# Performance work log

Hardware: AMD Instinct MI355X
Metric: run time of the kernel (lower is better)

The kernel has to match this reference:

```python
import jax, jax.numpy as jnp
import numpy as np

BN_EPS = 1e-5

def _sqdist(a, b):
    # a: (B,N,3), b: (B,M,3) -> (B,N,M)
    return (jnp.sum(a**2, -1)[:, :, None] + jnp.sum(b**2, -1)[:, None, :]
            - 2.0 * jnp.einsum('bnc,bmc->bnm', a, b))

def _knn_idx(pts, k):
    # smallest-k neighbor indices, (B,N,k)
    d = _sqdist(pts, pts)
    _, idx = jax.lax.top_k(-d, k)
    return idx

def _group(feat, idx):
    # feat (B,C,N), idx (B,N,K) -> (B,C,N,K)
    return jax.vmap(lambda f, i: f[:, i])(feat, idx)

def _gather_pts(pts, idx):
    # pts (B,M,C), idx (B,...) -> (B,...,C)
    return jax.vmap(lambda p, i: p[i])(pts, idx)

def _conv1(w, b, x):
    # 1x1 conv1d: w (O,C), x (B,C,N)
    return jnp.einsum('oc,bcn->bon', w, x) + b[None, :, None]

def _conv2(w, x, b=None):
    # 1x1 conv2d: w (O,C), x (B,C,N,K)
    y = jnp.einsum('oc,bcnk->bonk', w, x)
    return y if b is None else y + b[None, :, None, None]

def _bn_eval(x, gamma, beta):
    # eval-mode BatchNorm2d with running_mean=0, running_var=1
    s = gamma / jnp.sqrt(1.0 + BN_EPS)
    return x * s[None, :, None, None] + beta[None, :, None, None]

def _lgrp(x_q, x, P_anchor, map_idx, anchor_dist, lw1, lw2, lw3, k=16):
    # x_q, x: (B,n,3) -> weights (B,dim,n,k)
    d = _sqdist(x_q, x)
    _, idx = jax.lax.top_k(-d, k)                      # (B,n,k)
    neighbors = _gather_pts(x, idx)                    # (B,n,k,3)
    R1 = jnp.abs(x_q[:, :, None, :] - neighbors)       # (B,n,k,3)
    B_idx = _gather_pts(map_idx[..., None], idx)[..., 0]  # (B,n,k)
    anchorA = _gather_pts(P_anchor, map_idx)           # (B,n,3)
    anchorB = _gather_pts(P_anchor, B_idx)             # (B,n,k,3)
    dA = jnp.linalg.norm(x_q - anchorA, axis=-1)       # (B,n)
    dB = jnp.linalg.norm(neighbors - anchorB, axis=-1) # (B,n,k)
    dAB = jax.vmap(lambda ad, a, bi: ad[a[:, None], bi])(anchor_dist, map_idx, B_idx)
    R2s = dA[:, :, None] + dAB + dB                    # (B,n,k)
    R2 = jnp.broadcast_to(R2s[..., None], R1.shape)
    feats = jnp.concatenate([R1, R2], axis=-1).transpose(0, 3, 1, 2)  # (B,6,n,k)
    h = jax.nn.relu(_conv2(lw1, feats))
    h = jax.nn.relu(_conv2(lw2, h))
    return _conv2(lw3, h)                              # (B,dim,n,k)

def setup_inputs() -> dict:
    key = jax.random.key(0)
    ks = jax.random.split(key, 32)
    B, C_in, n, dim, M, k = 2, 128, 2048, 256, 128, 16
    hid_p, hid_a = 64, dim * 4
    s = 0.05
    inp = {
        'x': jax.random.normal(ks[0], (B, C_in, n), jnp.float32),
        'pos': jax.random.normal(ks[1], (B, 3, n), jnp.float32),
        'fps_idx': jax.random.randint(ks[2], (B, n), 0, n),
        'P_anchor': jax.random.normal(ks[3], (B, M, 3), jnp.float32),
        'map_idx': jax.random.randint(ks[4], (B, n), 0, M),
        'anchor_dist': jax.random.uniform(ks[5], (B, M, M), jnp.float32) * 2.0,
        'w_start': jax.random.normal(ks[6], (dim, C_in)) * s,
        'b_start': jnp.zeros((dim,), jnp.float32),
        'w_key': jax.random.normal(ks[7], (dim, dim)) * s,
        'b_key': jnp.zeros((dim,), jnp.float32),
        'w_query': jax.random.normal(ks[8], (dim, dim)) * s,
        'b_query': jnp.zeros((dim,), jnp.float32),
        'w_value': jax.random.normal(ks[9], (dim, dim)) * s,
        'b_value': jnp.zeros((dim,), jnp.float32),
        'pw1': jax.random.normal(ks[10], (hid_p, 3)) * s,
        'pb1': jnp.zeros((hid_p,), jnp.float32),
        'pg1': jnp.ones((hid_p,), jnp.float32),
        'pbt1': jnp.zeros((hid_p,), jnp.float32),
        'pw2': jax.random.normal(ks[11], (dim, hid_p)) * s,
        'pb2': jnp.zeros((dim,), jnp.float32),
        'lw1': jax.random.normal(ks[12], (32, 6)) * s,
        'lw2': jax.random.normal(ks[13], (64, 32)) * s,
        'lw3': jax.random.normal(ks[14], (dim, 64)) * s,
        'aw1': jax.random.normal(ks[15], (hid_a, dim)) * s,
        'ab1': jnp.zeros((hid_a,), jnp.float32),
        'ag1': jnp.ones((hid_a,), jnp.float32),
        'abt1': jnp.zeros((hid_a,), jnp.float32),
        'aw2': jax.random.normal(ks[16], (dim, hid_a)) * s,
        'ab2': jnp.zeros((dim,), jnp.float32),
        'w_end': jax.random.normal(ks[17], (C_in, dim)) * s,
        'b_end': jnp.zeros((C_in,), jnp.float32),
    }
    return inp

def reference(x, pos, fps_idx, P_anchor, map_idx, anchor_dist,
              w_start, b_start, w_key, b_key, w_query, b_query, w_value, b_value,
              pw1, pb1, pg1, pbt1, pw2, pb2, lw1, lw2, lw3,
              aw1, ab1, ag1, abt1, aw2, ab2, w_end, b_end):
    n_knn = 16
    identity = x
    xf = _conv1(w_start, b_start, x)                   # (B,dim,n)
    pos_f = pos.transpose(0, 2, 1)                     # (B,n,3)
    idx_knn = _knn_idx(pos_f, n_knn)                   # (B,n,k)
    key_f = _conv1(w_key, b_key, xf)
    value = _conv1(w_value, b_value, xf)
    query = _conv1(w_query, b_query, xf)
    key_g = _group(key_f, idx_knn)                     # (B,dim,n,k)
    qk_rel = query[:, :, :, None] - key_g
    pos_rel = pos[:, :, :, None] - _group(pos, idx_knn)
    f_l = _lgrp(pos_f, pos_f, P_anchor, map_idx, anchor_dist, lw1, lw2, lw3, k=16)
    # pos_mlp: conv-bn-relu-conv
    h = _bn_eval(_conv2(pw1, pos_rel, pb1), pg1, pbt1)
    pos_emb = _conv2(pw2, jax.nn.relu(h), pb2)         # (B,dim,n,k)
    # attn_mlp
    a = _bn_eval(_conv2(aw1, qk_rel + pos_emb + f_l, ab1), ag1, abt1)
    attention = _conv2(aw2, jax.nn.relu(a), ab2)
    attention = jax.nn.softmax(attention, axis=-1)
    value_e = value[:, :, :, None] + pos_emb + f_l
    agg = jnp.sum(attention * value_e, axis=-1)        # (B,dim,n)
    y = _conv1(w_end, b_end, agg)
    return y + identity
```

## Files before the change

kernel.cpp:

```cpp
#include <hip/hip_runtime.h>
#include <hip/hip_bf16.h>

typedef __hip_bfloat16 bf16;
typedef unsigned short u16;
typedef __attribute__((ext_vector_type(8))) short s8v;
typedef __attribute__((ext_vector_type(4))) float f32x4;

#define NP    2048
#define DC    256
#define MA    128
#define KNN_  16
#define LKV   768

#define MFMA_B16(a,b,c) __builtin_amdgcn_mfma_f32_16x16x32_bf16(a,b,c,0,0,0)

__device__ __forceinline__ float u2f(u16 u){ return __uint_as_float(((unsigned int)u)<<16); }
__device__ __forceinline__ u16 f2u(float f){ bf16 h=__float2bfloat16(f); u16 us; __builtin_memcpy(&us,&h,2); return us; }

__device__ __forceinline__ s8v ldpk(const u16* pk, int rb, int KS, int ks, int l){
  return *(const s8v*)(pk + (((size_t)((rb*KS + ks)*64 + l))<<3));
}

__device__ __forceinline__ s8v ldF(const u16* base, int cf, int ks, int NKS, int l){
  return *(const s8v*)((const char*)base + (((cf*NKS + ks)<<10) | (l<<4)));
}
__device__ __forceinline__ int faddr(int col, int ch, int NKS){
  int cf = col>>4, ks = ch>>5, lane = (((ch>>3)&3)<<4)|(col&15), j = ch&7;
  return ((cf*NKS + ks)<<10) + (lane<<4) + (j<<1);
}
__device__ __forceinline__ void stF4(u16* base, int col, int ch0, int NKS,
                                     float v0, float v1, float v2, float v3){
  uint2 pkv;
  pkv.x = (unsigned)f2u(v0) | ((unsigned)f2u(v1)<<16);
  pkv.y = (unsigned)f2u(v2) | ((unsigned)f2u(v3)<<16);
  *(uint2*)((char*)base + faddr(col, ch0, NKS)) = pkv;
}
__device__ __forceinline__ void stF1(u16* base, int col, int ch, int NKS, float v){
  *(u16*)((char*)base + faddr(col, ch, NKS)) = f2u(v);
}
__device__ __forceinline__ void ldF4(const u16* base, int col, int ch0, int NKS, float* o){
  uint2 pkv = *(const uint2*)((const char*)base + faddr(col, ch0, NKS));
  o[0] = u2f(pkv.x & 0xffff); o[1] = u2f(pkv.x>>16);
  o[2] = u2f(pkv.y & 0xffff); o[3] = u2f(pkv.y>>16);
}

template<bool XT, bool OT, bool RES>
__global__ __launch_bounds__(256) void mgemm(
    const u16* __restrict__ apk, const float* __restrict__ X,
    const float* __restrict__ bias, const float* __restrict__ resid,
    float* __restrict__ out, int M, int N, int K, int ldo)
{
  __shared__ u16 Bt[64*256];
  const int tid = threadIdx.x;
  const int w = tid>>6, l = tid&63, k = l&15, g = l>>4;
  const int n0 = blockIdx.x*64, m0 = blockIdx.y*128, bb = blockIdx.z;
  const int KS = K >> 5;
  if constexpr (!XT) {
    for (int e = tid*4; e < 64*K; e += 1024) {
      int kk = e >> 6, c = e & 63;
      float4 v = *(const float4*)(X + (size_t)bb*K*N + (size_t)kk*N + n0 + c);
      stF1(Bt, c+0, kk, KS, v.x); stF1(Bt, c+1, kk, KS, v.y);
      stF1(Bt, c+2, kk, KS, v.z); stF1(Bt, c+3, kk, KS, v.w);
    }
  } else {
    for (int e = tid*4; e < 64*256; e += 1024) {
      int c = e >> 8, kk = e & 255;
      float4 v = *(const float4*)(X + ((size_t)bb*N + n0 + c)*256 + kk);
      stF4(Bt, c, kk, KS, v.x, v.y, v.z, v.w);
    }
  }
  __syncthreads();
  f32x4 acc[2][4] = {};
  const int rbase = (m0>>4) + w*2;
  for (int ks = 0; ks < KS; ks++) {
    s8v a0 = ldpk(apk, rbase,   KS, ks, l);
    s8v a1 = ldpk(apk, rbase+1, KS, ks, l);
#pragma unroll
    for (int cf = 0; cf < 4; cf++) {
      s8v bF = ldF(Bt, cf, ks, KS, l);
      acc[0][cf] = MFMA_B16(a0, bF, acc[0][cf]);
      acc[1][cf] = MFMA_B16(a1, bF, acc[1][cf]);
    }
  }
#pragma unroll
  for (int ri = 0; ri < 2; ri++) {
    int mrow = m0 + w*32 + ri*16 + g*4;
#pragma unroll
    for (int r = 0; r < 4; r++) {
      int m = mrow + r;
      float bv = bias[m];
#pragma unroll
      for (int cf = 0; cf < 4; cf++) {
        int n = n0 + cf*16 + k;
        float v = acc[ri][cf][r] + bv;
        if constexpr (RES) v += resid[((size_t)bb*M + m)*N + n];
        if constexpr (OT) out[((size_t)bb*N + n)*ldo + m] = v;
        else              out[((size_t)bb*M + m)*N + n] = v;
      }
    }
  }
}

__global__ __launch_bounds__(1024) void knn_kernel(const float* __restrict__ pos, int* __restrict__ idx)
{
  __shared__ float px[NP], py[NP], pz[NP], pn[NP];
  const int tid = threadIdx.x;
  const int w = tid >> 6, l = tid & 63;
  const int bb = blockIdx.x >> 7;
  const int q0 = (blockIdx.x & 127) * 16;
  const float* pp = pos + (size_t)bb * 3 * NP;
  for (int t = tid; t < NP; t += 1024) {
    float x = pp[t], y = pp[NP + t], z = pp[2*NP + t];
    px[t] = x; py[t] = y; pz[t] = z; pn[t] = x*x + y*y + z*z;
  }
  __syncthreads();
  const int qi = q0 + w;
  const float qx = px[qi], qy = py[qi], qz = pz[qi], qn = pn[qi];
  float bd[16]; int bi[16];
#pragma unroll
  for (int t = 0; t < 16; t++) { bd[t] = 3.4e38f; bi[t] = -1; }
  float worst = 3.4e38f;
  for (int t = 0; t < 32; t++) {
    int j = t*64 + l;
    float d = qn + pn[j] - 2.f * (qx*px[j] + qy*py[j] + qz*pz[j]);
    if (__any(d < worst)) {
      float cd = (d < worst) ? d : 3.4e38f;
      int   cj = j;
#pragma unroll
      for (int s = 0; s < 16; s++) {
        bool sw = cd < bd[s];
        float od = bd[s]; int oj = bi[s];
        bd[s] = sw ? cd : od;  bi[s] = sw ? cj : oj;
        cd    = sw ? od : cd;  cj    = sw ? oj : cj;
      }
      worst = bd[15];
    }
  }
  int myj = 0;
#pragma unroll
  for (int r = 0; r < 16; r++) {
    float md = bd[0]; int mj = bi[0];
#pragma unroll
    for (int o = 1; o < 64; o <<= 1) {
      float od = __shfl_xor(md, o);
      int   oj = __shfl_xor(mj, o);
      bool tk = (od < md) || (od == md && ((unsigned)oj < (unsigned)mj));
      md = tk ? od : md;  mj = tk ? oj : mj;
    }
    if (l == r) myj = mj;
    bool win = (bi[0] == mj);
#pragma unroll
    for (int s = 0; s < 15; s++) {
      bd[s] = win ? bd[s+1] : bd[s];
      bi[s] = win ? bi[s+1] : bi[s];
    }
    bd[15] = win ? 3.4e38f : bd[15];
  }
  if (l < 16) idx[((size_t)bb * NP + qi) * KNN_ + l] = myj;
}

__global__ __launch_bounds__(256) void prep_kernel(
    const float* __restrict__ aw1, const float* __restrict__ aw2,
    const float* __restrict__ lw3, const float* __restrict__ pw2,
    const float* __restrict__ w_start, const float* __restrict__ w_key,
    const float* __restrict__ w_query, const float* __restrict__ w_value,
    const float* __restrict__ w_end,
    const float* __restrict__ b_key, const float* __restrict__ b_query,
    const float* __restrict__ b_value,
    const float* __restrict__ ag1, const float* __restrict__ ab1, const float* __restrict__ abt1,
    const float* __restrict__ pg1, const float* __restrict__ pb1, const float* __restrict__ pbt1,
    u16* __restrict__ aw1pk, u16* __restrict__ aw2pk, u16* __restrict__ wppk,
    u16* __restrict__ wstpk, u16* __restrict__ wkqvpk, u16* __restrict__ wendpk,
    float* __restrict__ sa, float* __restrict__ oa, float* __restrict__ sp,
    float* __restrict__ op_, float* __restrict__ bkqv)
{
  int i = blockIdx.x * 256 + threadIdx.x;
  const float inv = rsqrtf(1.0f + 1e-5f);
  if (i < 262144) {
    int rb = i >> 12, rem = i & 4095, ks = rem >> 9, l = (rem >> 3) & 63, j = rem & 7;
    int row = rb*16 + (l & 15), colk = ks*32 + (l >> 4)*8 + j;
    aw1pk[i] = f2u(aw1[(size_t)row*256 + colk]); return;
  }
  i -= 262144;
  if (i < 262144) {
    int rb = i >> 14, rem = i & 16383, ks = rem >> 9, l = (rem >> 3) & 63, j = rem & 7;
    int row = rb*16 + (l & 15), colk = ks*32 + (l >> 4)*8 + j;
    aw2pk[i] = f2u(aw2[(size_t)row*1024 + colk]); return;
  }
  i -= 262144;
  if (i < 32768) {
    int rb = i >> 11, rem = i & 2047, ks = rem >> 9, l = (rem >> 3) & 63, j = rem & 7;
    int row = rb*16 + (l & 15), colk = ks*32 + (l >> 4)*8 + j;
    float v = (colk < 64) ? lw3[row*64 + colk] : pw2[row*64 + (colk - 64)];
    wppk[i] = f2u(v); return;
  }
  i -= 32768;
  if (i < 32768) {
    int rb = i >> 11, rem = i & 2047, ks = rem >> 9, l = (rem >> 3) & 63, j = rem & 7;
    int row = rb*16 + (l & 15), colk = ks*32 + (l >> 4)*8 + j;
    wstpk[i] = f2u(w_start[(size_t)row*128 + colk]); return;
  }
  i -= 32768;
  if (i < 196608) {
    int rb = i >> 12, rem = i & 4095, ks = rem >> 9, l = (rem >> 3) & 63, j = rem & 7;
    int row = rb*16 + (l & 15), colk = ks*32 + (l >> 4)*8 + j;
    float v = (row < 256) ? w_key[(size_t)row*256 + colk]
            : (row < 512) ? w_query[(size_t)(row-256)*256 + colk]
                          : w_value[(size_t)(row-512)*256 + colk];
    wkqvpk[i] = f2u(v); return;
  }
  i -= 196608;
  if (i < 32768) {
    int rb = i >> 12, rem = i & 4095, ks = rem >> 9, l = (rem >> 3) & 63, j = rem & 7;
    int row = rb*16 + (l & 15), colk = ks*32 + (l >> 4)*8 + j;
    wendpk[i] = f2u(w_end[(size_t)row*256 + colk]); return;
  }
  i -= 32768;
  if (i < 1024) { float s_ = ag1[i]*inv; sa[i] = s_; oa[i] = ab1[i]*s_ + abt1[i]; return; }
  i -= 1024;
  if (i < 64)  { float s_ = pg1[i]*inv; sp[i] = s_; op_[i] = pb1[i]*s_ + pbt1[i]; return; }
  i -= 64;
  if (i < 768) {
    bkqv[i] = (i < 256) ? b_key[i] : (i < 512) ? b_query[i-256] : b_value[i-512];
  }
}

__global__ __launch_bounds__(256, 2) void fused_attn(
    const float* __restrict__ kqv, const int* __restrict__ knn_idx,
    const float* __restrict__ pos, const int* __restrict__ map_idx,
    const float* __restrict__ P_anchor, const float* __restrict__ adist,
    const float* __restrict__ lw1f, const float* __restrict__ lw2f, const float* __restrict__ pw1f,
    const float* __restrict__ spv, const float* __restrict__ opv, const float* __restrict__ pb2f,
    const u16* __restrict__ aw1pk, const float* __restrict__ sav, const float* __restrict__ oav,
    const u16* __restrict__ aw2pk, const u16* __restrict__ wppk, const float* __restrict__ ab2f,
    float* __restrict__ aggT)
{
  __shared__ __align__(16) char smem[65536];
  u16*   s_t   = (u16*)smem;
  u16*   hid0  = (u16*)(smem + 32768);
  u16*   hid1  = (u16*)(smem + 49152);
  float* fFEAT = (float*)smem;
  float* fPREL = (float*)(smem + 1632);
  u16*   fH1   = (u16*) (smem + 2448);

  const int tid = threadIdx.x;
  const int w = tid >> 6, l = tid & 63;
  const int k = l & 15, g = l >> 4;
  const int p0 = blockIdx.x * 4;
  const int b = p0 >> 11, pi0 = p0 & 2047;
  const int pi = pi0 + w;
  const int col_w = w*16 + k;

  const float* kqvB = kqv + (size_t)b * NP * LKV;
  const int* knnB = knn_idx + ((size_t)b * NP) * KNN_;

  if (l < 16) {
    int kk = l;
    int j = knnB[(size_t)pi * KNN_ + kk];
    const float* pp = pos + (size_t)b * 3 * NP;
    float qx = pp[pi], qy = pp[NP+pi], qz = pp[2*NP+pi];
    float nx = pp[j],  ny = pp[NP+j],  nz = pp[2*NP+j];
    float r1x = qx-nx, r1y = qy-ny, r1z = qz-nz;
    fPREL[(w*3+0)*17+kk] = r1x; fPREL[(w*3+1)*17+kk] = r1y; fPREL[(w*3+2)*17+kk] = r1z;
    int mi = map_idx[b*NP + pi];
    int bj = map_idx[b*NP + j];
    const float* pa = P_anchor + (size_t)b * MA * 3;
    float ax = pa[mi*3], ay = pa[mi*3+1], az = pa[mi*3+2];
    float bx = pa[bj*3], by = pa[bj*3+1], bz = pa[bj*3+2];
    float dA = sqrtf((qx-ax)*(qx-ax)+(qy-ay)*(qy-ay)+(qz-az)*(qz-az));
    float dB = sqrtf((nx-bx)*(nx-bx)+(ny-by)*(ny-by)+(nz-bz)*(nz-bz));
    float dAB = adist[(size_t)b*MA*MA + mi*MA + bj];
    float r2 = dA + dAB + dB;
    fFEAT[(w*6+0)*17+kk] = fabsf(r1x); fFEAT[(w*6+1)*17+kk] = fabsf(r1y);
    fFEAT[(w*6+2)*17+kk] = fabsf(r1z);
    fFEAT[(w*6+3)*17+kk] = r2; fFEAT[(w*6+4)*17+kk] = r2; fFEAT[(w*6+5)*17+kk] = r2;
  }
  __syncthreads();

  {
    float f0=fFEAT[(w*6+0)*17+k], f1=fFEAT[(w*6+1)*17+k], f2=fFEAT[(w*6+2)*17+k],
          f3=fFEAT[(w*6+3)*17+k], f4=fFEAT[(w*6+4)*17+k], f5=fFEAT[(w*6+5)*17+k];
#pragma unroll
    for (int jj = 0; jj < 8; jj++) {
      int h = g*8 + jj;
      const float* wp = lw1f + h*6;
      float v = wp[0]*f0 + wp[1]*f1 + wp[2]*f2 + wp[3]*f3 + wp[4]*f4 + wp[5]*f5;
      fH1[(w*32+h)*17+k] = f2u(fmaxf(v, 0.f));
    }
  }
  __syncthreads();

  {
    float hr[32];
#pragma unroll
    for (int t = 0; t < 32; t++) hr[t] = u2f(fH1[(w*32+t)*17+k]);
#pragma unroll
    for (int jj = 0; jj < 16; jj++) {
      int h = g*16 + jj;
      const float4* wp = (const float4*)(lw2f + h*32);
      float a = 0.f;
#pragma unroll
      for (int t4 = 0; t4 < 8; t4++) {
        float4 wv = wp[t4];
        a += wv.x*hr[t4*4] + wv.y*hr[t4*4+1] + wv.z*hr[t4*4+2] + wv.w*hr[t4*4+3];
      }
      stF1(hid0, col_w, h, 4, fmaxf(a, 0.f));
    }
    float pr0 = fPREL[(w*3+0)*17+k], pr1 = fPREL[(w*3+1)*17+k], pr2 = fPREL[(w*3+2)*17+k];
#pragma unroll
    for (int jj = 0; jj < 16; jj++) {
      int h = g*16 + jj;
      float d = pw1f[h*3]*pr0 + pw1f[h*3+1]*pr1 + pw1f[h*3+2]*pr2;
      stF1(hid0, col_w, 64 + h, 4, fmaxf(d*spv[h] + opv[h], 0.f));
    }
  }
  __syncthreads();

  {
    f32x4 accs[4][4];
#pragma unroll
    for (int fr = 0; fr < 4; fr++) {
      int ch0 = w*64 + fr*16 + g*4;
      const float4 p4 = *(const float4*)(pb2f + ch0);
#pragma unroll
      for (int fc = 0; fc < 4; fc++) {
        int j = knnB[(size_t)(pi0 + fc) * KNN_ + k];
        const float4 q4 = *(const float4*)(kqvB + (size_t)(pi0 + fc)*LKV + 256 + ch0);
        const float4 k4 = *(const float4*)(kqvB + (size_t)j*LKV + ch0);
        accs[fr][fc][0] = q4.x - k4.x + p4.x;
        accs[fr][fc][1] = q4.y - k4.y + p4.y;
        accs[fr][fc][2] = q4.z - k4.z + p4.z;
        accs[fr][fc][3] = q4.w - k4.w + p4.w;
      }
    }
#pragma unroll
    for (int ks = 0; ks < 4; ks++) {
      s8v aF[4];
#pragma unroll
      for (int fr = 0; fr < 4; fr++) aF[fr] = ldpk(wppk, w*4 + fr, 4, ks, l);
#pragma unroll
      for (int fc = 0; fc < 4; fc++) {
        s8v bF = ldF(hid0, fc, ks, 4, l);
#pragma unroll
        for (int fr = 0; fr < 4; fr++) accs[fr][fc] = MFMA_B16(aF[fr], bF, accs[fr][fc]);
      }
    }
#pragma unroll
    for (int fr = 0; fr < 4; fr++)
#pragma unroll
      for (int fc = 0; fc < 4; fc++)
        stF4(s_t, fc*16 + k, w*64 + fr*16 + g*4, 8,
             accs[fr][fc][0], accs[fr][fc][1], accs[fr][fc][2], accs[fr][fc][3]);
  }
  __syncthreads();

  f32x4 acc2[4][4];
#pragma unroll
  for (int fr = 0; fr < 4; fr++) {
    const float4 a4 = *(const float4*)(ab2f + w*64 + fr*16 + g*4);
#pragma unroll
    for (int fc = 0; fc < 4; fc++) {
      acc2[fr][fc][0] = a4.x; acc2[fr][fc][1] = a4.y;
      acc2[fr][fc][2] = a4.z; acc2[fr][fc][3] = a4.w;
    }
  }

  {
    f32x4 acc1[2][4] = {};
    const int rb0 = w*2;
#pragma unroll
    for (int ks = 0; ks < 8; ks++) {
      s8v a0 = ldpk(aw1pk, rb0,     8, ks, l);
      s8v a1 = ldpk(aw1pk, rb0 + 1, 8, ks, l);
#pragma unroll
      for (int cf = 0; cf < 4; cf++) {
        s8v bF = ldF(s_t, cf, ks, 8, l);
        acc1[0][cf] = MFMA_B16(a0, bF, acc1[0][cf]);
        acc1[1][cf] = MFMA_B16(a1, bF, acc1[1][cf]);
      }
    }
#pragma unroll
    for (int ri = 0; ri < 2; ri++) {
      int hl = w*32 + ri*16 + g*4;
      const float4 sc = *(const float4*)(sav + hl);
      const float4 of = *(const float4*)(oav + hl);
#pragma unroll
      for (int cf = 0; cf < 4; cf++) {
        float v0 = fmaxf(acc1[ri][cf][0]*sc.x + of.x, 0.f);
        float v1 = fmaxf(acc1[ri][cf][1]*sc.y + of.y, 0.f);
        float v2 = fmaxf(acc1[ri][cf][2]*sc.z + of.z, 0.f);
        float v3 = fmaxf(acc1[ri][cf][3]*sc.w + of.w, 0.f);
        stF4(hid0, cf*16 + k, hl, 4, v0, v1, v2, v3);
      }
    }
  }
  __syncthreads();

  for (int c = 0; c < 8; c++) {
    u16* cur = (c & 1) ? hid1 : hid0;
    u16* nxt = (c & 1) ? hid0 : hid1;
#pragma unroll
    for (int ks = 0; ks < 4; ks++) {
      s8v aF[4];
#pragma unroll
      for (int rf = 0; rf < 4; rf++) aF[rf] = ldpk(aw2pk, w*4 + rf, 32, c*4 + ks, l);
#pragma unroll
      for (int cf = 0; cf < 4; cf++) {
        s8v bF = ldF(cur, cf, ks, 4, l);
#pragma unroll
        for (int rf = 0; rf < 4; rf++) acc2[rf][cf] = MFMA_B16(aF[rf], bF, acc2[rf][cf]);
      }
    }
    if (c < 7) {
      f32x4 acc1[2][4] = {};
      const int rb0 = (c+1)*8 + w*2;
#pragma unroll
      for (int ks = 0; ks < 8; ks++) {
        s8v a0 = ldpk(aw1pk, rb0,     8, ks, l);
        s8v a1 = ldpk(aw1pk, rb0 + 1, 8, ks, l);
#pragma unroll
        for (int cf = 0; cf < 4; cf++) {
          s8v bF = ldF(s_t, cf, ks, 8, l);
          acc1[0][cf] = MFMA_B16(a0, bF, acc1[0][cf]);
          acc1[1][cf] = MFMA_B16(a1, bF, acc1[1][cf]);
        }
      }
#pragma unroll
      for (int ri = 0; ri < 2; ri++) {
        int hl = w*32 + ri*16 + g*4;
        int hg = (c+1)*128 + hl;
        const float4 sc = *(const float4*)(sav + hg);
        const float4 of = *(const float4*)(oav + hg);
#pragma unroll
        for (int cf = 0; cf < 4; cf++) {
          float v0 = fmaxf(acc1[ri][cf][0]*sc.x + of.x, 0.f);
          float v1 = fmaxf(acc1[ri][cf][1]*sc.y + of.y, 0.f);
          float v2 = fmaxf(acc1[ri][cf][2]*sc.z + of.z, 0.f);
          float v3 = fmaxf(acc1[ri][cf][3]*sc.w + of.w, 0.f);
          stF4(nxt, cf*16 + k, hl, 4, v0, v1, v2, v3);
        }
      }
      __syncthreads();
    }
  }

#pragma unroll
  for (int fc = 0; fc < 4; fc++) {
    int j = knnB[(size_t)(pi0 + fc) * KNN_ + k];
    const float* qp = kqvB + (size_t)(pi0 + fc)*LKV + 256;
    const float* kp = kqvB + (size_t)j*LKV;
    const float* vp = kqvB + (size_t)(pi0 + fc)*LKV + 512;
#pragma unroll
    for (int fr = 0; fr < 4; fr++) {
      int ch0 = w*64 + fr*16 + g*4;
      float q4[4], k4[4], v4[4], s4[4], res[4];
      *(float4*)q4 = *(const float4*)(qp + ch0);
      *(float4*)k4 = *(const float4*)(kp + ch0);
      *(float4*)v4 = *(const float4*)(vp + ch0);
      ldF4(s_t, fc*16 + k, ch0, 8, s4);
#pragma unroll
      for (int r = 0; r < 4; r++) {
        float a = acc2[fr][fc][r];
        float m = a;
        m = fmaxf(m, __shfl_xor(m, 1, 16)); m = fmaxf(m, __shfl_xor(m, 2, 16));
        m = fmaxf(m, __shfl_xor(m, 4, 16)); m = fmaxf(m, __shfl_xor(m, 8, 16));
        float ex = __expf(a - m);
        float se = ex;
        se += __shfl_xor(se, 1, 16); se += __shfl_xor(se, 2, 16);
        se += __shfl_xor(se, 4, 16); se += __shfl_xor(se, 8, 16);
        float watt = ex / se;
        float ve = v4[r] - q4[r] + k4[r] + s4[r];
        float cc = watt * ve;
        cc += __shfl_xor(cc, 1, 16); cc += __shfl_xor(cc, 2, 16);
        cc += __shfl_xor(cc, 4, 16); cc += __shfl_xor(cc, 8, 16);
        res[r] = cc;
      }
      if (k == 0)
        *(float4*)(aggT + ((size_t)(b*NP) + pi0 + fc)*DC + ch0) =
            make_float4(res[0], res[1], res[2], res[3]);
    }
  }
}

extern "C" void kernel_launch(void* const* d_in, const int* in_sizes, int n_in,
                              void* d_out, int out_size, void* d_ws, size_t ws_size,
                              hipStream_t stream)
{
  const float* x        = (const float*)d_in[0];
  const float* pos      = (const float*)d_in[1];
  const float* P_anchor = (const float*)d_in[3];
  const int*   map_idx  = (const int*)  d_in[4];
  const float* adist    = (const float*)d_in[5];
  const float* w_start  = (const float*)d_in[6];
  const float* b_start  = (const float*)d_in[7];
  const float* w_key    = (const float*)d_in[8];
  const float* b_key    = (const float*)d_in[9];
  const float* w_query  = (const float*)d_in[10];
  const float* b_query  = (const float*)d_in[11];
  const float* w_value  = (const float*)d_in[12];
  const float* b_value  = (const float*)d_in[13];
  const float* pw1      = (const float*)d_in[14];
  const float* pb1      = (const float*)d_in[15];
  const float* pg1      = (const float*)d_in[16];
  const float* pbt1     = (const float*)d_in[17];
  const float* pw2      = (const float*)d_in[18];
  const float* pb2      = (const float*)d_in[19];
  const float* lw1      = (const float*)d_in[20];
  const float* lw2      = (const float*)d_in[21];
  const float* lw3      = (const float*)d_in[22];
  const float* aw1      = (const float*)d_in[23];
  const float* ab1      = (const float*)d_in[24];
  const float* ag1      = (const float*)d_in[25];
  const float* abt1     = (const float*)d_in[26];
  const float* aw2      = (const float*)d_in[27];
  const float* ab2      = (const float*)d_in[28];
  const float* w_end    = (const float*)d_in[29];
  const float* b_end    = (const float*)d_in[30];

  if (ws_size < (size_t)4672384 * 4) return;

  float* ws     = (float*)d_ws;
  float* xf     = ws + 0;
  float* aggT   = ws + 0;
  float* kqvT   = ws + 1048576;
  u16*   aw1pk  = (u16*)(ws + 4194304);
  u16*   aw2pk  = (u16*)(ws + 4325376);
  u16*   wppk   = (u16*)(ws + 4456448);
  u16*   wstpk  = (u16*)(ws + 4472832);
  u16*   wkqvpk = (u16*)(ws + 4489216);
  u16*   wendpk = (u16*)(ws + 4587520);
  float* sa     = ws + 4603904;
  float* oa     = ws + 4604928;
  float* sp     = ws + 4605952;
  float* op_    = ws + 4606016;
  float* bkqv   = ws + 4606080;
  int*   knn_i  = (int*)(ws + 4606848);

  prep_kernel<<<3208, 256, 0, stream>>>(aw1, aw2, lw3, pw2,
      w_start, w_key, w_query, w_value, w_end, b_key, b_query, b_value,
      ag1, ab1, abt1, pg1, pb1, pbt1,
      aw1pk, aw2pk, wppk, wstpk, wkqvpk, wendpk, sa, oa, sp, op_, bkqv);

  mgemm<false, false, false><<<dim3(32, 2, 2), 256, 0, stream>>>(
      wstpk, x, b_start, nullptr, xf, 256, NP, 128, 0);

  knn_kernel<<<256, 1024, 0, stream>>>(pos, knn_i);

  mgemm<false, true, false><<<dim3(32, 6, 2), 256, 0, stream>>>(
      wkqvpk, xf, bkqv, nullptr, kqvT, 768, NP, 256, LKV);

  fused_attn<<<1024, 256, 0, stream>>>(kqvT, knn_i,
      pos, map_idx, P_anchor, adist,
      lw1, lw2, pw1, sp, op_, pb2,
      aw1pk, sa, oa, aw2pk, wppk, ab2, aggT);

  mgemm<true, false, true><<<dim3(32, 1, 2), 256, 0, stream>>>(
      wendpk, aggT, b_end, x, (float*)d_out, 128, NP, 256, 0);
}
```

Measured before the change: 224.7 us.

## Fuse start conv into KQV projection and raise wave priority around MFMA loops

Adds a kqv_fused kernel that computes the start 1x1 conv (x -> xf) in shared memory and feeds it straight into the key/query/value projection. This removes one kernel launch and the global round trip of xf. In exchange, each of the 6 row-blocks recomputes the start conv for its column tile, which is redundant compute, and the intermediate is rounded to bf16 in LDS. It also wraps the MFMA loops in fused_attn with s_setprio(1)/(0) so waves issuing matrix ops get scheduling priority.

```diff
diff --git a/kernel.cpp b/kernel.cpp
--- a/kernel.cpp
+++ b/kernel.cpp
@@ -42,6 +42,84 @@
   uint2 pkv = *(const uint2*)((const char*)base + faddr(col, ch0, NKS));
   o[0] = u2f(pkv.x & 0xffff); o[1] = u2f(pkv.x>>16);
   o[2] = u2f(pkv.y & 0xffff); o[3] = u2f(pkv.y>>16);
+}
+
+__global__ __launch_bounds__(256) void kqv_fused(
+    const u16* __restrict__ wstpk, const float* __restrict__ b_start,
+    const u16* __restrict__ wkqvpk, const float* __restrict__ bkqv,
+    const float* __restrict__ x, float* __restrict__ kqvT)
+{
+  __shared__ u16 Bx[64*128];
+  __shared__ u16 Bt[64*256];
+  const int tid = threadIdx.x;
+  const int w = tid>>6, l = tid&63, k = l&15, g = l>>4;
+  const int n0 = blockIdx.x*64, m0 = blockIdx.y*128, bb = blockIdx.z;
+  for (int e = tid*4; e < 64*128; e += 1024) {
+    int kk = e >> 6, c = e & 63;
+    float4 v = *(const float4*)(x + (size_t)bb*128*NP + (size_t)kk*NP + n0 + c);
+    stF1(Bx, c+0, kk, 4, v.x); stF1(Bx, c+1, kk, 4, v.y);
+    stF1(Bx, c+2, kk, 4, v.z); stF1(Bx, c+3, kk, 4, v.w);
+  }
+  __syncthreads();
+  {
+    f32x4 accx[4][4];
+#pragma unroll
+    for (int fr = 0; fr < 4; fr++) {
+      int ch0 = w*64 + fr*16 + g*4;
+      float4 b4 = *(const float4*)(b_start + ch0);
+#pragma unroll
+      for (int cf = 0; cf < 4; cf++) {
+        accx[fr][cf][0] = b4.x; accx[fr][cf][1] = b4.y;
+        accx[fr][cf][2] = b4.z; accx[fr][cf][3] = b4.w;
+      }
+    }
+#pragma unroll
+    for (int ks = 0; ks < 4; ks++) {
+      s8v aF[4];
+#pragma unroll
+      for (int fr = 0; fr < 4; fr++) aF[fr] = ldpk(wstpk, w*4 + fr, 4, ks, l);
+#pragma unroll
+      for (int cf = 0; cf < 4; cf++) {
+        s8v bF = ldF(Bx, cf, ks, 4, l);
+#pragma unroll
+        for (int fr = 0; fr < 4; fr++) accx[fr][cf] = MFMA_B16(aF[fr], bF, accx[fr][cf]);
+      }
+    }
+#pragma unroll
+    for (int fr = 0; fr < 4; fr++)
+#pragma unroll
+      for (int cf = 0; cf < 4; cf++)
+        stF4(Bt, cf*16 + k, w*64 + fr*16 + g*4, 8,
+             accx[fr][cf][0], accx[fr][cf][1], accx[fr][cf][2], accx[fr][cf][3]);
+  }
+  __syncthreads();
+  f32x4 acc[2][4] = {};
+  const int rbase = (m0>>4) + w*2;
+#pragma unroll
+  for (int ks = 0; ks < 8; ks++) {
+    s8v a0 = ldpk(wkqvpk, rbase,   8, ks, l);
+    s8v a1 = ldpk(wkqvpk, rbase+1, 8, ks, l);
+#pragma unroll
+    for (int cf = 0; cf < 4; cf++) {
+      s8v bF = ldF(Bt, cf, ks, 8, l);
+      acc[0][cf] = MFMA_B16(a0, bF, acc[0][cf]);
+      acc[1][cf] = MFMA_B16(a1, bF, acc[1][cf]);
+    }
+  }
+#pragma unroll
+  for (int ri = 0; ri < 2; ri++) {
+    int mrow = m0 + w*32 + ri*16 + g*4;
+#pragma unroll
+    for (int r = 0; r < 4; r++) {
+      int m = mrow + r;
+      float bv = bkqv[m];
+#pragma unroll
+      for (int cf = 0; cf < 4; cf++) {
+        int n = n0 + cf*16 + k;
+        kqvT[((size_t)bb*NP + n)*LKV + m] = acc[ri][cf][r] + bv;
+      }
+    }
+  }
 }
 
 template<bool XT, bool OT, bool RES>
@@ -368,6 +446,7 @@
   {
     f32x4 acc1[2][4] = {};
     const int rb0 = w*2;
+    __builtin_amdgcn_s_setprio(1);
 #pragma unroll
     for (int ks = 0; ks < 8; ks++) {
       s8v a0 = ldpk(aw1pk, rb0,     8, ks, l);
@@ -379,6 +458,7 @@
         acc1[1][cf] = MFMA_B16(a1, bF, acc1[1][cf]);
       }
     }
+    __builtin_amdgcn_s_setprio(0);
 #pragma unroll
     for (int ri = 0; ri < 2; ri++) {
       int hl = w*32 + ri*16 + g*4;
@@ -399,6 +479,7 @@
   for (int c = 0; c < 8; c++) {
     u16* cur = (c & 1) ? hid1 : hid0;
     u16* nxt = (c & 1) ? hid0 : hid1;
+    __builtin_amdgcn_s_setprio(1);
 #pragma unroll
     for (int ks = 0; ks < 4; ks++) {
       s8v aF[4];
@@ -411,9 +492,11 @@
         for (int rf = 0; rf < 4; rf++) acc2[rf][cf] = MFMA_B16(aF[rf], bF, acc2[rf][cf]);
       }
     }
+    __builtin_amdgcn_s_setprio(0);
     if (c < 7) {
       f32x4 acc1[2][4] = {};
       const int rb0 = (c+1)*8 + w*2;
+      __builtin_amdgcn_s_setprio(1);
 #pragma unroll
       for (int ks = 0; ks < 8; ks++) {
         s8v a0 = ldpk(aw1pk, rb0,     8, ks, l);
@@ -425,6 +508,7 @@
           acc1[1][cf] = MFMA_B16(a1, bF, acc1[1][cf]);
         }
       }
+      __builtin_amdgcn_s_setprio(0);
 #pragma unroll
       for (int ri = 0; ri < 2; ri++) {
         int hl = w*32 + ri*16 + g*4;
@@ -520,7 +604,6 @@
   if (ws_size < (size_t)4672384 * 4) return;
 
   float* ws     = (float*)d_ws;
-  float* xf     = ws + 0;
   float* aggT   = ws + 0;
   float* kqvT   = ws + 1048576;
   u16*   aw1pk  = (u16*)(ws + 4194304);
@@ -541,13 +624,10 @@
       ag1, ab1, abt1, pg1, pb1, pbt1,
       aw1pk, aw2pk, wppk, wstpk, wkqvpk, wendpk, sa, oa, sp, op_, bkqv);
 
-  mgemm<false, false, false><<<dim3(32, 2, 2), 256, 0, stream>>>(
-      wstpk, x, b_start, nullptr, xf, 256, NP, 128, 0);
-
   knn_kernel<<<256, 1024, 0, stream>>>(pos, knn_i);
 
-  mgemm<false, true, false><<<dim3(32, 6, 2), 256, 0, stream>>>(
-      wkqvpk, xf, bkqv, nullptr, kqvT, 768, NP, 256, LKV);
+  kqv_fused<<<dim3(32, 6, 2), 256, 0, stream>>>(
+      wstpk, b_start, wkqvpk, bkqv, x, kqvT);
 
   fused_attn<<<1024, 256, 0, stream>>>(kqvT, knn_i,
       pos, map_idx, P_anchor, adist,
```

Measured after the change: 209.2 us. 1.07x faster.
